# Kernel tuning notes

Hardware: AMD Instinct MI355X
Metric: run time of the kernel (lower is better)

The kernel has to match this reference:

```python
import jax, jax.numpy as jnp
import numpy as np


def _combos(n, k):
    # all n-tuples of nonnegative ints summing to k, same order as the torch module
    if n == 1:
        yield (k,)
        return
    for i in range(k + 1):
        for t in _combos(n - 1, k - i):
            yield (i,) + t


def _make_exponents(action_dim, rank):
    rows = []
    for total in range(rank + 1):
        rows.extend(_combos(action_dim, total))
    # [action_dim, num_basis], matching the registered buffer exponents.T layout
    return np.asarray(rows, dtype=np.int32).T


def setup_inputs() -> dict:
    key = jax.random.key(0)
    action_dim, rank, batch = 8, 4, 131072
    actions = jax.random.normal(key, (batch, action_dim), dtype=jnp.float32)
    exponents = jnp.asarray(_make_exponents(action_dim, rank))  # [D, NB], NB=495
    return {"actions": actions, "exponents": exponents, "rank": rank}


def reference(actions, exponents, rank):
    # actions: [B, D] float; exponents: [D, NB] int32; rank: python int
    x = jnp.clip(actions, -1.0, 1.0)  # [B, D]
    # Legendre recurrence P_n(x) = ((2n-1)/n) x P_{n-1}(x) - ((n-1)/n) P_{n-2}(x)
    polys = [jnp.ones_like(x)]
    if rank >= 1:
        polys.append(x)
    for n in range(2, rank + 1):
        polys.append(((2.0 * n - 1.0) / n) * x * polys[-1] - ((n - 1.0) / n) * polys[-2])
    P = jnp.stack(polys, axis=-1)  # [B, D, rank+1]
    # gather the needed order per (dimension, basis function) and multiply over dims
    idx = jnp.broadcast_to(exponents[None, :, :], (x.shape[0],) + exponents.shape)  # [B, D, NB]
    gathered = jnp.take_along_axis(P, idx.astype(jnp.int32), axis=2)  # [B, D, NB]
    return jnp.prod(gathered, axis=1)  # [B, NB]
```

## Files before the change

### kernel.cpp

```cpp
#include <hip/hip_runtime.h>
#include <math.h>


#define THREADS 256
#define TILE 32
#define ROWSTRIDE 41

typedef float f32x4 __attribute__((ext_vector_type(4)));

__global__ __launch_bounds__(THREADS, 8) void legendre_fast(
    const float* __restrict__ actions,
    const int* __restrict__ exps,
    float* __restrict__ out,
    int B, int D, int NB, int rank, int stepq, int stepr)
{
    __shared__ unsigned prog[512];
    __shared__ float Pl[TILE * ROWSTRIDE];

    const int t = threadIdx.x;
    const int r0 = blockIdx.x * TILE;

    for (int nb = t; nb < NB; nb += THREADS) {
        unsigned pk = 0;
        int shift = 0;
        for (int d = 0; d < D; ++d) {
            int e = exps[d * NB + nb];
            if (e > 0) {
                pk |= (unsigned)(d * 5 + e) << shift;
                shift += 6;
            }
        }
        prog[((nb & 3) << 7) | (nb >> 2)] = pk;
    }

    if (t < TILE * D) {
        int rl = t / D;
        int d  = t - rl * D;
        float x = actions[(long long)(r0 + rl) * D + d];
        x = fminf(fmaxf(x, -1.0f), 1.0f);
        float* Pr = &Pl[rl * ROWSTRIDE + d * 5];
        float p0 = 1.0f, p1 = x;
        Pr[0] = 1.0f;
        if (rank >= 1) Pr[1] = x;
        for (int n = 2; n <= rank; ++n) {
            float fn = (float)n;
            float pn = ((2.0f * fn - 1.0f) / fn) * x * p1
                     - ((fn - 1.0f) / fn) * p0;
            Pr[n] = pn;
            p0 = p1;
            p1 = pn;
        }
    }
    __syncthreads();

    const int nchunks = (TILE * NB) >> 2;
    f32x4* __restrict__ o4 = (f32x4*)(out + (long long)r0 * NB);

    int o0 = t << 2;
    int rl = o0 / NB;
    int nb = o0 - rl * NB;

    for (int c = t; c < nchunks; c += THREADS) {
        int nbi = nb, rli = rl;
        float res[4];
#pragma unroll
        for (int i = 0; i < 4; ++i) {
            unsigned pk = prog[((nbi & 3) << 7) | (nbi >> 2)];
            const float* Pr = &Pl[rli * ROWSTRIDE];
            float f0 = Pr[pk & 63u];
            float f1 = Pr[(pk >> 6) & 63u];
            float f2 = Pr[(pk >> 12) & 63u];
            float f3 = Pr[(pk >> 18) & 63u];
            res[i] = (f0 * f1) * (f2 * f3);
            ++nbi;
            if (nbi == NB) { nbi = 0; ++rli; }
        }
        f32x4 v;
        v.x = res[0]; v.y = res[1]; v.z = res[2]; v.w = res[3];
        __builtin_nontemporal_store(v, o4 + c);

        nb += stepr;
        rl += stepq;
        if (nb >= NB) { nb -= NB; ++rl; }
    }
}

__global__ void legendre_generic(
    const float* __restrict__ actions,
    const int* __restrict__ exps,
    float* __restrict__ out,
    long long total, int D, int NB)
{
    long long stride = (long long)gridDim.x * blockDim.x;
    for (long long i = (long long)blockIdx.x * blockDim.x + threadIdx.x;
         i < total; i += stride) {
        int nb = (int)(i % NB);
        long long row = i / NB;
        float prod = 1.0f;
        for (int d = 0; d < D; ++d) {
            int e = exps[d * NB + nb];
            float x = actions[row * D + d];
            x = fminf(fmaxf(x, -1.0f), 1.0f);
            float p0 = 1.0f, p1 = x;
            float p = (e == 0) ? 1.0f : x;
            for (int n = 2; n <= e; ++n) {
                float fn = (float)n;
                float pn = ((2.0f * fn - 1.0f) / fn) * x * p1
                         - ((fn - 1.0f) / fn) * p0;
                p0 = p1;
                p1 = pn;
                p = pn;
            }
            prod *= p;
        }
        out[i] = prod;
    }
}

extern "C" void kernel_launch(void* const* d_in, const int* in_sizes, int n_in,
                              void* d_out, int out_size, void* d_ws, size_t ws_size,
                              hipStream_t stream) {
    const float* actions = (const float*)d_in[0];
    const int* exps = (const int*)d_in[1];
    float* out = (float*)d_out;

    long long in0 = in_sizes[0];
    long long in1 = in_sizes[1];
    long long osz = out_size;

    int D = (int)(sqrt((double)in0 * (double)in1 / (double)osz) + 0.5);
    if (D < 1) D = 1;
    int NB = (int)(in1 / D);
    int B = (int)(in0 / D);

    int rank = -1;
    {
        long long c = 1;
        for (int r = 0; r <= 32; ++r) {
            if (c == (long long)NB) { rank = r; break; }
            c = c * (D + r + 1) / (r + 1);
            if (c > (long long)NB) break;
        }
    }

    bool fast = (rank >= 0 && rank <= 4 && D >= 1 && D <= 8 &&
                 NB >= 1 && NB <= 512 &&
                 (long long)B * NB == osz && (long long)B * D == in0 &&
                 (B % TILE) == 0 && ((TILE * NB) % 4) == 0);

    if (fast) {
        int nblk = B / TILE;
        int stepq = (THREADS * 4) / NB;
        int stepr = (THREADS * 4) % NB;
        legendre_fast<<<nblk, THREADS, 0, stream>>>(
            actions, exps, out, B, D, NB, rank, stepq, stepr);
    } else {
        long long total = osz;
        long long want = (total + 255) / 256;
        int nblk = (want > 8192) ? 8192 : (int)(want > 0 ? want : 1);
        legendre_generic<<<nblk, 256, 0, stream>>>(
            actions, exps, out, total, D, NB);
    }
}
```

Baseline: 55.42 us.

## Factor basis into two 4-dim half-products, each output one multiply of two LDS lookups

Each row's 8-dim basis product is split into two halves over dims 0-3 and 4-7. Each half has 70 combinations of total degree at most 4, so those partial products are precomputed per row into LDS. Every output then needs two LDS reads and one multiply instead of four reads and three multiplies. The per-basis program becomes a pair of combinatorial ranks, packed four at a time into a 64-bit word with row-wrap flags. The fast path is now specialised to D=8 and NB=495, the non-temporal store becomes a normal store, and launch bounds drop to 4 waves. Shared memory per block grows, which may reduce occupancy.

```diff
diff --git a/kernel.cpp b/kernel.cpp
--- a/kernel.cpp
+++ b/kernel.cpp
@@ -4,84 +4,126 @@
 
 #define THREADS 256
 #define TILE 32
-#define ROWSTRIDE 41
+#define RSTRIDE 142
 
 typedef float f32x4 __attribute__((ext_vector_type(4)));
 
-__global__ __launch_bounds__(THREADS, 8) void legendre_fast(
+__device__ __forceinline__ int c2i(int n){ return (n < 2) ? 0 : (n*(n-1))>>1; }
+__device__ __forceinline__ int c3i(int n){ return (n < 3) ? 0 : (n*(n-1)*(n-2))/6; }
+__device__ __forceinline__ int c4i(int n){ return (n < 4) ? 0 : (n*(n-1)*(n-2)*(n-3))/24; }
+
+__device__ __forceinline__ int rank4(int a, int b, int c, int d) {
+    return (70 - c4i(8-a)) + (c3i(7-a) - c3i(7-a-b))
+         + (c2i(6-a-b) - c2i(6-a-b-c)) + d;
+}
+
+__global__ __launch_bounds__(THREADS, 4) void legendre_fast(
     const float* __restrict__ actions,
     const int* __restrict__ exps,
-    float* __restrict__ out,
-    int B, int D, int NB, int rank, int stepq, int stepr)
+    float* __restrict__ out)
 {
-    __shared__ unsigned prog[512];
-    __shared__ float Pl[TILE * ROWSTRIDE];
+    __shared__ unsigned long long cprog[495];
+    __shared__ float UV[TILE * RSTRIDE];
+    __shared__ unsigned short tmp16[496];
 
     const int t = threadIdx.x;
     const int r0 = blockIdx.x * TILE;
 
-    for (int nb = t; nb < NB; nb += THREADS) {
-        unsigned pk = 0;
-        int shift = 0;
-        for (int d = 0; d < D; ++d) {
-            int e = exps[d * NB + nb];
-            if (e > 0) {
-                pk |= (unsigned)(d * 5 + e) << shift;
-                shift += 6;
+    for (int nb = t; nb < 495; nb += THREADS) {
+        int e0 = exps[0*495+nb], e1 = exps[1*495+nb];
+        int e2 = exps[2*495+nb], e3 = exps[3*495+nb];
+        int e4 = exps[4*495+nb], e5 = exps[5*495+nb];
+        int e6 = exps[6*495+nb], e7 = exps[7*495+nb];
+        int ai = rank4(e0, e1, e2, e3);
+        int bi = rank4(e4, e5, e6, e7);
+        tmp16[nb] = (unsigned short)(ai | (bi << 7));
+    }
+    __syncthreads();
+
+    if (t < 64) {
+        int row = t >> 1, half = t & 1;
+        f32x4 xv = *(const f32x4*)(actions + (long long)(r0 + row) * 8 + half * 4);
+        float P[4][5];
+#pragma unroll
+        for (int d = 0; d < 4; ++d) {
+            float x = fminf(fmaxf(xv[d], -1.0f), 1.0f);
+            P[d][0] = 1.0f; P[d][1] = x;
+#pragma unroll
+            for (int n = 2; n <= 4; ++n) {
+                float fn = (float)n;
+                P[d][n] = ((2.0f*fn - 1.0f)/fn) * x * P[d][n-1]
+                        - ((fn - 1.0f)/fn) * P[d][n-2];
             }
         }
-        prog[((nb & 3) << 7) | (nb >> 2)] = pk;
-    }
-
-    if (t < TILE * D) {
-        int rl = t / D;
-        int d  = t - rl * D;
-        float x = actions[(long long)(r0 + rl) * D + d];
-        x = fminf(fmaxf(x, -1.0f), 1.0f);
-        float* Pr = &Pl[rl * ROWSTRIDE + d * 5];
-        float p0 = 1.0f, p1 = x;
-        Pr[0] = 1.0f;
-        if (rank >= 1) Pr[1] = x;
-        for (int n = 2; n <= rank; ++n) {
-            float fn = (float)n;
-            float pn = ((2.0f * fn - 1.0f) / fn) * x * p1
-                     - ((fn - 1.0f) / fn) * p0;
-            Pr[n] = pn;
-            p0 = p1;
-            p1 = pn;
+        float* W = &UV[row * RSTRIDE + half * 71];
+        int cnt = 0;
+#pragma unroll
+        for (int a = 0; a <= 4; ++a) { float q0 = P[0][a];
+#pragma unroll
+            for (int b = 0; b <= 4-a; ++b) { float q1 = q0 * P[1][b];
+#pragma unroll
+                for (int c = 0; c <= 4-a-b; ++c) { float q2 = q1 * P[2][c];
+#pragma unroll
+                    for (int d = 0; d <= 4-a-b-c; ++d) { W[cnt++] = q2 * P[3][d]; }
+                }
+            }
+        }
+    } else {
+        for (int j = t - 64; j < 495; j += THREADS - 64) {
+            int f = 4 * j;
+            int nb0 = f;
+            nb0 -= (nb0 >= 990) ? 990 : 0;
+            nb0 -= (nb0 >= 495) ? 495 : 0;
+            unsigned p0 = tmp16[nb0];
+            int n1 = nb0 + 1; unsigned w1 = (n1 >= 495); n1 -= w1 ? 495 : 0;
+            int n2 = nb0 + 2; unsigned w2 = (n2 >= 495); n2 -= w2 ? 495 : 0;
+            int n3 = nb0 + 3; unsigned w3 = (n3 >= 495); n3 -= w3 ? 495 : 0;
+            unsigned p1 = tmp16[n1], p2 = tmp16[n2], p3 = tmp16[n3];
+            unsigned lo = p0 | (p1 << 14) | (w1 << 28) | (w2 << 29) | (w3 << 30);
+            unsigned hi = p2 | (p3 << 14);
+            cprog[j] = ((unsigned long long)hi << 32) | lo;
         }
     }
     __syncthreads();
 
-    const int nchunks = (TILE * NB) >> 2;
-    f32x4* __restrict__ o4 = (f32x4*)(out + (long long)r0 * NB);
+    const int nchunks = TILE * 495 / 4;
+    f32x4* __restrict__ o4 = (f32x4*)(out + (long long)r0 * 495);
 
-    int o0 = t << 2;
-    int rl = o0 / NB;
-    int nb = o0 - rl * NB;
+    int m = t;
+    int f0 = 4 * t;
+    int rl = (f0 >= 495) + (f0 >= 990);
+    int nb0 = f0 - rl * 495;
+    int rowoff = rl * RSTRIDE;
 
     for (int c = t; c < nchunks; c += THREADS) {
-        int nbi = nb, rli = rl;
-        float res[4];
-#pragma unroll
-        for (int i = 0; i < 4; ++i) {
-            unsigned pk = prog[((nbi & 3) << 7) | (nbi >> 2)];
-            const float* Pr = &Pl[rli * ROWSTRIDE];
-            float f0 = Pr[pk & 63u];
-            float f1 = Pr[(pk >> 6) & 63u];
-            float f2 = Pr[(pk >> 12) & 63u];
-            float f3 = Pr[(pk >> 18) & 63u];
-            res[i] = (f0 * f1) * (f2 * f3);
-            ++nbi;
-            if (nbi == NB) { nbi = 0; ++rli; }
+        unsigned long long e = cprog[m];
+        unsigned lo = (unsigned)e, hi = (unsigned)(e >> 32);
+        float r0v, r1v, r2v, r3v;
+        {
+            int a = lo & 127, b = (lo >> 7) & 127;
+            r0v = UV[rowoff + a] * UV[rowoff + 71 + b];
         }
-        f32x4 v;
-        v.x = res[0]; v.y = res[1]; v.z = res[2]; v.w = res[3];
-        __builtin_nontemporal_store(v, o4 + c);
+        {
+            int a = (lo >> 14) & 127, b = (lo >> 21) & 127;
+            int ro = rowoff + (((lo >> 28) & 1) ? RSTRIDE : 0);
+            r1v = UV[ro + a] * UV[ro + 71 + b];
+        }
+        {
+            int a = hi & 127, b = (hi >> 7) & 127;
+            int ro = rowoff + (((lo >> 29) & 1) ? RSTRIDE : 0);
+            r2v = UV[ro + a] * UV[ro + 71 + b];
+        }
+        {
+            int a = (hi >> 14) & 127, b = (hi >> 21) & 127;
+            int ro = rowoff + (((lo >> 30) & 1) ? RSTRIDE : 0);
+            r3v = UV[ro + a] * UV[ro + 71 + b];
+        }
+        f32x4 v; v.x = r0v; v.y = r1v; v.z = r2v; v.w = r3v;
+        o4[c] = v;
 
-        nb += stepr;
-        rl += stepq;
-        if (nb >= NB) { nb -= NB; ++rl; }
+        m += THREADS; if (m >= 495) m -= 495;
+        nb0 += 34; rowoff += 2 * RSTRIDE;
+        if (nb0 >= 495) { nb0 -= 495; rowoff += RSTRIDE; }
     }
 }
 
@@ -105,11 +147,8 @@
             float p = (e == 0) ? 1.0f : x;
             for (int n = 2; n <= e; ++n) {
                 float fn = (float)n;
-                float pn = ((2.0f * fn - 1.0f) / fn) * x * p1
-                         - ((fn - 1.0f) / fn) * p0;
-                p0 = p1;
-                p1 = pn;
-                p = pn;
+                float pn = ((2.0f*fn - 1.0f)/fn) * x * p1 - ((fn - 1.0f)/fn) * p0;
+                p0 = p1; p1 = pn; p = pn;
             }
             prod *= p;
         }
@@ -133,27 +172,12 @@
     int NB = (int)(in1 / D);
     int B = (int)(in0 / D);
 
-    int rank = -1;
-    {
-        long long c = 1;
-        for (int r = 0; r <= 32; ++r) {
-            if (c == (long long)NB) { rank = r; break; }
-            c = c * (D + r + 1) / (r + 1);
-            if (c > (long long)NB) break;
-        }
-    }
-
-    bool fast = (rank >= 0 && rank <= 4 && D >= 1 && D <= 8 &&
-                 NB >= 1 && NB <= 512 &&
+    bool fast = (D == 8 && NB == 495 &&
                  (long long)B * NB == osz && (long long)B * D == in0 &&
-                 (B % TILE) == 0 && ((TILE * NB) % 4) == 0);
+                 (B % TILE) == 0);
 
     if (fast) {
-        int nblk = B / TILE;
-        int stepq = (THREADS * 4) / NB;
-        int stepr = (THREADS * 4) % NB;
-        legendre_fast<<<nblk, THREADS, 0, stream>>>(
-            actions, exps, out, B, D, NB, rank, stepq, stepr);
+        legendre_fast<<<B / TILE, THREADS, 0, stream>>>(actions, exps, out);
     } else {
         long long total = osz;
         long long want = (total + 255) / 256;
```

Result: faster. 46.90 us (-15.4%).
